# Performance work log

Measured on AMD Instinct MI355X. Metric: run time of the kernel, lower is better.

Reference implementation:

```python
import jax, jax.numpy as jnp
import numpy as np

V, E, L, H, C, NC = 32000, 128, 256, 2048, 256, 10   # vocab, embed, seq_len, ae_hidden, cnn_out/d_model, classes
D_INNER, D_STATE, DT_RANK, D_CONV = 512, 16, 16, 4    # mamba defaults for d_model=256 (expand=2)
B = 64


def setup_inputs() -> dict:
    key = jax.random.key(0)
    ks = jax.random.split(key, 20)
    def rn(k, shape, s=0.02):
        return jax.random.normal(k, shape, jnp.float32) * s
    return {
        "x": jax.random.randint(ks[0], (B, L), 0, V),
        "embed": rn(ks[1], (V, E), 1.0),
        "enc_w1": rn(ks[2], (H, E * L)), "enc_b1": jnp.zeros((H,), jnp.float32),
        "enc_w2": rn(ks[3], (E * L, H)), "enc_b2": jnp.zeros((E * L,), jnp.float32),
        "conv_w": rn(ks[4], (C, E, 5)), "conv_b": jnp.zeros((C,), jnp.float32),
        "in_proj_w": rn(ks[5], (2 * D_INNER, C)),
        "conv1d_w": rn(ks[6], (D_INNER, 1, D_CONV)), "conv1d_b": jnp.zeros((D_INNER,), jnp.float32),
        "x_proj_w": rn(ks[7], (DT_RANK + 2 * D_STATE, D_INNER)),
        "dt_proj_w": rn(ks[8], (D_INNER, DT_RANK), 0.1),
        "dt_proj_b": rn(ks[9], (D_INNER,), 0.1),
        "A_log": jnp.log(jnp.broadcast_to(jnp.arange(1, D_STATE + 1, dtype=jnp.float32), (D_INNER, D_STATE))),
        "D": jnp.ones((D_INNER,), jnp.float32),
        "out_proj_w": rn(ks[10], (C, D_INNER)),
        "fc_w": rn(ks[11], (NC, C)), "fc_b": jnp.zeros((NC,), jnp.float32),
    }


def _mamba(xs, in_proj_w, conv1d_w, conv1d_b, x_proj_w, dt_proj_w, dt_proj_b, A_log, Dp, out_proj_w):
    # xs: (B, Lp, C)
    xz = xs @ in_proj_w.T                                   # (B, Lp, 2*d_inner)
    u, z = jnp.split(xz, 2, axis=-1)
    # causal depthwise conv1d + SiLU
    u_c = u.transpose(0, 2, 1)                              # (B, d_inner, Lp)
    u_c = jnp.pad(u_c, ((0, 0), (0, 0), (D_CONV - 1, 0)))
    u_c = jax.lax.conv_general_dilated(
        u_c, conv1d_w, window_strides=(1,), padding=[(0, 0)],
        dimension_numbers=("NCH", "OIH", "NCH"), feature_group_count=D_INNER)
    u = jax.nn.silu((u_c + conv1d_b[None, :, None]).transpose(0, 2, 1))  # (B, Lp, d_inner)
    # input-dependent dt, B, C
    xdbl = u @ x_proj_w.T
    dt, Bm, Cm = jnp.split(xdbl, [DT_RANK, DT_RANK + D_STATE], axis=-1)
    delta = jax.nn.softplus(dt @ dt_proj_w.T + dt_proj_b)   # (B, Lp, d_inner)
    A = -jnp.exp(A_log)                                     # (d_inner, d_state)
    dA = jnp.exp(jnp.einsum("bld,dn->bldn", delta, A))      # (B, Lp, d_inner, d_state)
    dBu = (delta * u)[..., None] * Bm[:, :, None, :]        # (B, Lp, d_inner, d_state)
    # sequential selective scan over time
    def step(h, inp):
        dA_t, dBu_t, c_t = inp
        h = dA_t * h + dBu_t                                # (B, d_inner, d_state)
        y = jnp.einsum("bdn,bn->bd", h, c_t)
        return h, y
    h0 = jnp.zeros((xs.shape[0], D_INNER, D_STATE), xs.dtype)
    _, ys = jax.lax.scan(step, h0, (dA.transpose(1, 0, 2, 3), dBu.transpose(1, 0, 2, 3), Cm.transpose(1, 0, 2)))
    y = ys.transpose(1, 0, 2) + u * Dp                      # (B, Lp, d_inner)
    y = y * jax.nn.silu(z)
    return y @ out_proj_w.T                                 # (B, Lp, C)


def reference(x, embed, enc_w1, enc_b1, enc_w2, enc_b2, conv_w, conv_b,
              in_proj_w, conv1d_w, conv1d_b, x_proj_w, dt_proj_w, dt_proj_b,
              A_log, D, out_proj_w, fc_w, fc_b):
    b = x.shape[0]
    e = embed[x].reshape(b, -1)                             # (B, E*L)
    h = jax.nn.relu(e @ enc_w1.T + enc_b1)
    h = jax.nn.relu(h @ enc_w2.T + enc_b2)
    h = h.reshape(b, L, E).transpose(0, 2, 1)               # (B, E, L)
    h = jax.lax.conv_general_dilated(h, conv_w, window_strides=(1,), padding=[(2, 2)],
                                     dimension_numbers=("NCH", "OIH", "NCH"))
    h = jax.nn.relu(h + conv_b[None, :, None])              # (B, C, L)
    h = h.reshape(b, C, L // 2, 2).max(axis=-1)             # MaxPool1d(2)
    xs = h.transpose(0, 2, 1)                               # (B, L/2, C)
    y = _mamba(xs, in_proj_w, conv1d_w, conv1d_b, x_proj_w, dt_proj_w, dt_proj_b, A_log, D, out_proj_w)
    return y.mean(axis=1) @ fc_w.T + fc_b                   # (B, NC)
```

## Files before the change

### kernel.cpp

```cpp
#include <hip/hip_runtime.h>
#include <cstddef>
#include <cstdint>

#define B_   64
#define L_   256
#define E_   128
#define H_   2048
#define C_   256
#define LP_  128
#define DI_  512
#define DS_  16

typedef __attribute__((ext_vector_type(8))) short s16x8;
typedef __attribute__((ext_vector_type(4))) float f32x4;

__device__ __forceinline__ uint32_t cvt_pk_bf16(float a, float b) {
  uint32_t r;
  asm("v_cvt_pk_bf16_f32 %0, %1, %2" : "=v"(r) : "v"(a), "v"(b));
  return r;
}

__device__ __forceinline__ void split1(float x, short& h, short& l) {
  uint32_t p = cvt_pk_bf16(x, x);
  float rres = x - __uint_as_float(p << 16);
  uint32_t q = cvt_pk_bf16(rres, rres);
  h = (short)p; l = (short)q;
}

__device__ __forceinline__ void cvt8(const float4& a0, const float4& a1,
                                     s16x8& h, s16x8& l) {
  union { uint32_t u[4]; s16x8 v; } H, L;
  float x[8] = {a0.x, a0.y, a0.z, a0.w, a1.x, a1.y, a1.z, a1.w};
#pragma unroll
  for (int j = 0; j < 4; ++j) {
    uint32_t p = cvt_pk_bf16(x[2*j], x[2*j+1]);
    float r0 = x[2*j]   - __uint_as_float(p << 16);
    float r1 = x[2*j+1] - __uint_as_float(p & 0xFFFF0000u);
    H.u[j] = p;
    L.u[j] = cvt_pk_bf16(r0, r1);
  }
  h = H.v; l = L.v;
}

__global__ __launch_bounds__(256) void embed_k(const int* __restrict__ x,
                                               const float* __restrict__ emb,
                                               short* __restrict__ ehi,
                                               short* __restrict__ elo) {
  int bl = blockIdx.x * 4 + (threadIdx.x >> 6);
  int lane = threadIdx.x & 63;
  int idx = x[bl];
  float2 v = ((const float2*)(emb + (size_t)idx * E_))[lane];
  uint32_t p = cvt_pk_bf16(v.x, v.y);
  float r0 = v.x - __uint_as_float(p << 16);
  float r1 = v.y - __uint_as_float(p & 0xFFFF0000u);
  uint32_t q = cvt_pk_bf16(r0, r1);
  ((uint32_t*)ehi)[(size_t)bl * 64 + lane] = p;
  ((uint32_t*)elo)[(size_t)bl * 64 + lane] = q;
}

__global__ __launch_bounds__(256) void prep_all(
    const float* __restrict__ conv_w, const float* __restrict__ ipw,
    const float* __restrict__ opw,    const float* __restrict__ xpw,
    short* __restrict__ wthi,  short* __restrict__ wtlo,
    short* __restrict__ ipwhi, short* __restrict__ ipwlo,
    short* __restrict__ opwhi, short* __restrict__ opwlo,
    short* __restrict__ xpwhi, short* __restrict__ xpwlo) {
  int blk = blockIdx.x, tid = threadIdx.x;
  if (blk < 640) {
    int k = blk, c = tid, t = k >> 7, e = k & 127;
    float v = conv_w[c * 640 + e * 5 + t];
    short h, l; split1(v, h, l);
    wthi[(size_t)c * 640 + k] = h; wtlo[(size_t)c * 640 + k] = l;
  } else if (blk < 640 + 1024) {
    int n = blk - 640;
    size_t i = (size_t)n * 256 + tid;
    short h, l; split1(ipw[i], h, l);
    ipwhi[i] = h; ipwlo[i] = l;
  } else if (blk < 640 + 1024 + 512) {
    size_t i = (size_t)(blk - 1664) * 256 + tid;
    short h, l; split1(opw[i], h, l);
    opwhi[i] = h; opwlo[i] = l;
  } else {
    int i = (blk - 2176) * 256 + tid;
    int n = i >> 9, k = i & 511;
    float v = (n < 48) ? xpw[n * 512 + k] : 0.0f;
    short h, l; split1(v, h, l);
    xpwhi[i] = h; xpwlo[i] = l;
  }
}

template<int AM, int WM, int EPI>
__global__ __launch_bounds__(256) void gemm_t(
    const void* __restrict__ Aa, const void* __restrict__ Ab,
    const void* __restrict__ Wa, const void* __restrict__ Wb,
    const float* __restrict__ bias,
    float* __restrict__ Cf, short* __restrict__ Chi, short* __restrict__ Clo,
    int M, int N, int K, int kChunk) {
  __shared__ __align__(16) short AhiS[64][40];
  __shared__ __align__(16) short AloS[64][40];
  __shared__ __align__(16) short WhiS[64][40];
  __shared__ __align__(16) short WloS[64][40];

  const int tid = threadIdx.x;
  const int r   = tid >> 2;
  const int seg = (tid & 3) * 8;
  const int lane = tid & 63;
  const int wv   = tid >> 6;
  const int ml   = lane & 15;
  const int quad = lane >> 4;
  const int bn = blockIdx.x * 64, bm = blockIdx.y * 64;
  const int kStart = blockIdx.z * kChunk, kEnd = kStart + kChunk;

  f32x4 acc[4];
#pragma unroll
  for (int nt = 0; nt < 4; ++nt) acc[nt] = (f32x4){0.f, 0.f, 0.f, 0.f};

  auto loadA = [&](int k0, s16x8& h, s16x8& l) {
    if constexpr (AM == 0) {
      const float* Ar = (const float*)Aa + (size_t)(bm + r) * K + seg + k0;
      float4 a0 = *(const float4*)Ar;
      float4 a1 = *(const float4*)(Ar + 4);
      cvt8(a0, a1, h, l);
    } else if constexpr (AM == 1) {
      size_t o = (size_t)(bm + r) * K + seg + k0;
      h = *(const s16x8*)((const short*)Aa + o);
      l = *(const s16x8*)((const short*)Ab + o);
    } else {
      int m = bm + r, bb = m >> 8, lrow = m & 255;
      int k = k0 + seg, t = k >> 7, e = k & 127;
      int ls = lrow + t - 2;
      if (ls >= 0 && ls < 256) {
        size_t o = ((size_t)bb << 15) + ((size_t)ls << 7) + (size_t)e;
        h = *(const s16x8*)((const short*)Aa + o);
        l = *(const s16x8*)((const short*)Ab + o);
      } else {
        h = (s16x8)(short)0; l = (s16x8)(short)0;
      }
    }
  };
  auto loadW = [&](int k0, s16x8& h, s16x8& l) {
    if constexpr (WM == 0) {
      const float* Wr = (const float*)Wa + (size_t)(bn + r) * K + seg + k0;
      float4 w0 = *(const float4*)Wr;
      float4 w1 = *(const float4*)(Wr + 4);
      cvt8(w0, w1, h, l);
    } else {
      size_t o = (size_t)(bn + r) * K + seg + k0;
      h = *(const s16x8*)((const short*)Wa + o);
      l = *(const s16x8*)((const short*)Wb + o);
    }
  };

  s16x8 pAh, pAl, pWh, pWl;
  loadA(kStart, pAh, pAl);
  loadW(kStart, pWh, pWl);

  for (int k0 = kStart; k0 < kEnd; k0 += 32) {
    __syncthreads();
    *(s16x8*)&AhiS[r][seg] = pAh;
    *(s16x8*)&AloS[r][seg] = pAl;
    *(s16x8*)&WhiS[r][seg] = pWh;
    *(s16x8*)&WloS[r][seg] = pWl;
    __syncthreads();
    if (k0 + 32 < kEnd) {
      loadA(k0 + 32, pAh, pAl);
      loadW(k0 + 32, pWh, pWl);
    }
    s16x8 fah = *(const s16x8*)&AhiS[wv * 16 + ml][quad * 8];
    s16x8 fal = *(const s16x8*)&AloS[wv * 16 + ml][quad * 8];
#pragma unroll
    for (int nt = 0; nt < 4; ++nt) {
      s16x8 fwh = *(const s16x8*)&WhiS[nt * 16 + ml][quad * 8];
      s16x8 fwl = *(const s16x8*)&WloS[nt * 16 + ml][quad * 8];
      acc[nt] = __builtin_amdgcn_mfma_f32_16x16x32_bf16(fah, fwh, acc[nt], 0, 0, 0);
      acc[nt] = __builtin_amdgcn_mfma_f32_16x16x32_bf16(fah, fwl, acc[nt], 0, 0, 0);
      acc[nt] = __builtin_amdgcn_mfma_f32_16x16x32_bf16(fal, fwh, acc[nt], 0, 0, 0);
    }
  }

  if constexpr (EPI == 1) {
    float* P = Cf + (size_t)blockIdx.z * ((size_t)M * N);
#pragma unroll
    for (int nt = 0; nt < 4; ++nt) {
      int n = bn + nt * 16 + ml;
#pragma unroll
      for (int i = 0; i < 4; ++i) {
        int m = bm + wv * 16 + quad * 4 + i;
        P[(size_t)m * N + n] = acc[nt][i];
      }
    }
  } else if constexpr (EPI == 0) {
#pragma unroll
    for (int nt = 0; nt < 4; ++nt) {
      int n = bn + nt * 16 + ml;
      float bv = bias ? bias[n] : 0.0f;
#pragma unroll
      for (int i = 0; i < 4; ++i) {
        int m = bm + wv * 16 + quad * 4 + i;
        Cf[(size_t)m * N + n] = acc[nt][i] + bv;
      }
    }
  } else if constexpr (EPI == 2) {
#pragma unroll
    for (int nt = 0; nt < 4; ++nt) {
      int n = bn + nt * 16 + ml;
      float bv = bias[n];
#pragma unroll
      for (int i = 0; i < 4; ++i) {
        int m = bm + wv * 16 + quad * 4 + i;
        float v = acc[nt][i] + bv;
        v = v > 0.0f ? v : 0.0f;
        short hh, ll; split1(v, hh, ll);
        Chi[(size_t)m * N + n] = hh;
        Clo[(size_t)m * N + n] = ll;
      }
    }
  } else {
    int m0 = bm + wv * 16 + quad * 4;
    int bb = m0 >> 8;
    int lb = m0 & 255;
    size_t row0 = ((size_t)bb * 128 + (lb >> 1)) * 256;
#pragma unroll
    for (int nt = 0; nt < 4; ++nt) {
      int n = bn + nt * 16 + ml;
      float bv = bias[n];
      float v0 = fmaxf(acc[nt][0] + bv, 0.0f);
      float v1 = fmaxf(acc[nt][1] + bv, 0.0f);
      float v2 = fmaxf(acc[nt][2] + bv, 0.0f);
      float v3 = fmaxf(acc[nt][3] + bv, 0.0f);
      float p0 = fmaxf(v0, v1), p1 = fmaxf(v2, v3);
      short hh, ll;
      split1(p0, hh, ll);
      Chi[row0 + n] = hh; Clo[row0 + n] = ll;
      split1(p1, hh, ll);
      Chi[row0 + 256 + n] = hh; Clo[row0 + 256 + n] = ll;
    }
  }
}

__global__ __launch_bounds__(256) void reduce_k(const float* __restrict__ P,
                                                const float* __restrict__ bias,
                                                short* __restrict__ hhi,
                                                short* __restrict__ hlo,
                                                int MN, int N, int S) {
  int i = blockIdx.x * 256 + threadIdx.x;
  if (i >= MN) return;
  float s = 0.0f;
  for (int z = 0; z < S; ++z) s += P[(size_t)z * MN + i];
  s += bias[i & (N - 1)];
  s = s > 0.0f ? s : 0.0f;
  short hh, ll; split1(s, hh, ll);
  hhi[i] = hh; hlo[i] = ll;
}

__global__ __launch_bounds__(512) void dwconv_k(const float* __restrict__ xz,
                                                const float* __restrict__ cw,
                                                const float* __restrict__ cb,
                                                float* __restrict__ u2) {
  int m = blockIdx.x;
  int t = m & (LP_ - 1);
  int d = threadIdx.x;
  float4 w = *(const float4*)(cw + d * 4);
  const float* base = xz + (size_t)m * (2 * DI_) + d;
  float pre = cb[d];
  if (t >= 3) {
    pre = fmaf(base[-3 * 2 * DI_], w.x, pre);
    pre = fmaf(base[-2 * 2 * DI_], w.y, pre);
    pre = fmaf(base[-1 * 2 * DI_], w.z, pre);
    pre = fmaf(base[0],            w.w, pre);
  } else {
    const float wv[4] = {w.x, w.y, w.z, w.w};
    for (int j = 0; j < 4; ++j) {
      int tt = t - 3 + j;
      if (tt >= 0) pre = fmaf(base[(j - 3) * 2 * DI_], wv[j], pre);
    }
  }
  float s = pre / (1.0f + __expf(-pre));
  u2[(size_t)m * DI_ + d] = s;
}

__global__ __launch_bounds__(256) void scan_k(const float* __restrict__ u2,
                                              const float* __restrict__ xz,
                                              const float* __restrict__ xdbl,
                                              const float* __restrict__ dtw,
                                              const float* __restrict__ dtb,
                                              const float* __restrict__ A_log,
                                              const float* __restrict__ Dp,
                                              short* __restrict__ yghi,
                                              short* __restrict__ yglo) {
  __shared__ float dls[16][128];
  const int tid = threadIdx.x;
  const int b = blockIdx.x >> 5;
  const int d0 = (blockIdx.x & 31) << 4;
  const size_t mBase = (size_t)b * LP_;

  {
    const int ch = tid >> 4;
    const int t0 = (tid & 15) * 8;
    const int d = d0 + ch;
    const float4* wr = (const float4*)(dtw + d * 16);
    float4 w0 = wr[0], w1 = wr[1], w2 = wr[2], w3 = wr[3];
    float bdt = dtb[d];
#pragma unroll
    for (int j = 0; j < 8; ++j) {
      int t = t0 + j;
      const float4* xr = (const float4*)(xdbl + (mBase + t) * 64);
      float4 x0 = xr[0], x1 = xr[1], x2 = xr[2], x3 = xr[3];
      float a = bdt;
      a = fmaf(w0.x, x0.x, a); a = fmaf(w0.y, x0.y, a);
      a = fmaf(w0.z, x0.z, a); a = fmaf(w0.w, x0.w, a);
      a = fmaf(w1.x, x1.x, a); a = fmaf(w1.y, x1.y, a);
      a = fmaf(w1.z, x1.z, a); a = fmaf(w1.w, x1.w, a);
      a = fmaf(w2.x, x2.x, a); a = fmaf(w2.y, x2.y, a);
      a = fmaf(w2.z, x2.z, a); a = fmaf(w2.w, x2.w, a);
      a = fmaf(w3.x, x3.x, a); a = fmaf(w3.y, x3.y, a);
      a = fmaf(w3.z, x3.z, a); a = fmaf(w3.w, x3.w, a);
      float sp = fmaxf(a, 0.0f) + log1pf(__expf(-fabsf(a)));
      dls[ch][t] = sp;
    }
  }
  __syncthreads();

  const int n = tid & 15;
  const int ch = tid >> 4;
  const int d = d0 + ch;
  float An = -__expf(A_log[d * 16 + n]);
  float Dd = Dp[d];
  float h = 0.0f;
  for (int t = 0; t < LP_; ++t) {
    size_t m = mBase + t;
    float dl = dls[ch][t];
    float uu = u2[m * DI_ + d];
    float Bn = xdbl[m * 64 + 16 + n];
    float Cn = xdbl[m * 64 + 32 + n];
    float dA = __expf(dl * An);
    h = fmaf(dA, h, (dl * uu) * Bn);
    float y = h * Cn;
    y += __shfl_xor(y, 1, 16);
    y += __shfl_xor(y, 2, 16);
    y += __shfl_xor(y, 4, 16);
    y += __shfl_xor(y, 8, 16);
    if (n == 0) {
      float zz = xz[m * (2 * DI_) + DI_ + d];
      float g = zz / (1.0f + __expf(-zz));
      float yv = fmaf(uu, Dd, y) * g;
      short hh, ll; split1(yv, hh, ll);
      yghi[m * DI_ + d] = hh;
      yglo[m * DI_ + d] = ll;
    }
  }
}

__global__ __launch_bounds__(256) void meanfc_k(const float* __restrict__ mout,
                                                const float* __restrict__ fcw,
                                                const float* __restrict__ fcb,
                                                float* __restrict__ out) {
  __shared__ float pooled[256];
  int b = blockIdx.x;
  int c = threadIdx.x;
  float s = 0.0f;
  for (int t = 0; t < LP_; ++t) s += mout[((size_t)b * LP_ + t) * C_ + c];
  pooled[c] = s * (1.0f / 128.0f);
  __syncthreads();
  if (c < 10) {
    float acc = fcb[c];
    for (int k = 0; k < 256; ++k) acc = fmaf(pooled[k], fcw[c * 256 + k], acc);
    out[b * 10 + c] = acc;
  }
}

extern "C" void kernel_launch(void* const* d_in, const int* in_sizes, int n_in,
                              void* d_out, int out_size, void* d_ws, size_t ws_size,
                              hipStream_t stream) {
  const int*   x         = (const int*)d_in[0];
  const float* embed     = (const float*)d_in[1];
  const float* enc_w1    = (const float*)d_in[2];
  const float* enc_b1    = (const float*)d_in[3];
  const float* enc_w2    = (const float*)d_in[4];
  const float* enc_b2    = (const float*)d_in[5];
  const float* conv_w    = (const float*)d_in[6];
  const float* conv_b    = (const float*)d_in[7];
  const float* in_proj_w = (const float*)d_in[8];
  const float* conv1d_w  = (const float*)d_in[9];
  const float* conv1d_b  = (const float*)d_in[10];
  const float* x_proj_w  = (const float*)d_in[11];
  const float* dt_proj_w = (const float*)d_in[12];
  const float* dt_proj_b = (const float*)d_in[13];
  const float* A_log     = (const float*)d_in[14];
  const float* Dp        = (const float*)d_in[15];
  const float* out_proj_w= (const float*)d_in[16];
  const float* fc_w      = (const float*)d_in[17];
  const float* fc_b      = (const float*)d_in[18];
  float* out = (float*)d_out;

  char* ws = (char*)d_ws;
  size_t off = 0;
  auto alloc = [&](size_t bytes) {
    char* p = ws + off;
    off += (bytes + 255) & ~(size_t)255;
    return p;
  };
  short* ehi   = (short*)alloc(2097152ull * 2);
  short* elo   = (short*)alloc(2097152ull * 2);
  float* P     = (float*)alloc(4194304ull * 4);
  short* h1hi  = (short*)alloc(131072ull  * 2);
  short* h1lo  = (short*)alloc(131072ull  * 2);
  short* h2hi  = (short*)alloc(2097152ull * 2);
  short* h2lo  = (short*)alloc(2097152ull * 2);
  short* wthi  = (short*)alloc(163840ull  * 2);
  short* wtlo  = (short*)alloc(163840ull  * 2);
  short* ipwhi = (short*)alloc(262144ull  * 2);
  short* ipwlo = (short*)alloc(262144ull  * 2);
  short* xpwhi = (short*)alloc(32768ull   * 2);
  short* xpwlo = (short*)alloc(32768ull   * 2);
  short* opwhi = (short*)alloc(131072ull  * 2);
  short* opwlo = (short*)alloc(131072ull  * 2);
  short* xshi  = (short*)alloc(2097152ull * 2);
  short* xslo  = (short*)alloc(2097152ull * 2);
  float* xz    = (float*)alloc(8388608ull * 4);
  float* u2    = (float*)alloc(4194304ull * 4);
  float* xdbl  = (float*)alloc(524288ull  * 4);
  short* yghi  = (short*)alloc(4194304ull * 2);
  short* yglo  = (short*)alloc(4194304ull * 2);
  float* mout  = (float*)alloc(2097152ull * 4);
  (void)ws_size; (void)in_sizes; (void)n_in; (void)out_size;

  prep_all<<<2304, 256, 0, stream>>>(conv_w, in_proj_w, out_proj_w, x_proj_w,
                                     wthi, wtlo, ipwhi, ipwlo, opwhi, opwlo,
                                     xpwhi, xpwlo);
  embed_k<<<4096, 256, 0, stream>>>(x, embed, ehi, elo);

  gemm_t<1, 0, 1><<<dim3(32, 1, 32), 256, 0, stream>>>(
      ehi, elo, enc_w1, nullptr, nullptr, P, nullptr, nullptr,
      64, 2048, 32768, 1024);
  reduce_k<<<512, 256, 0, stream>>>(P, enc_b1, h1hi, h1lo, 131072, 2048, 32);

  gemm_t<1, 0, 2><<<dim3(512, 1, 1), 256, 0, stream>>>(
      h1hi, h1lo, enc_w2, nullptr, enc_b2, nullptr, h2hi, h2lo,
      64, 32768, 2048, 2048);

  gemm_t<2, 1, 3><<<dim3(4, 256, 1), 256, 0, stream>>>(
      h2hi, h2lo, wthi, wtlo, conv_b, nullptr, xshi, xslo,
      16384, 256, 640, 640);

  gemm_t<1, 1, 0><<<dim3(16, 128, 1), 256, 0, stream>>>(
      xshi, xslo, ipwhi, ipwlo, nullptr, xz, nullptr, nullptr,
      8192, 1024, 256, 256);

  dwconv_k<<<8192, 512, 0, stream>>>(xz, conv1d_w, conv1d_b, u2);

  gemm_t<0, 1, 0><<<dim3(1, 128, 1), 256, 0, stream>>>(
      u2, nullptr, xpwhi, xpwlo, nullptr, xdbl, nullptr, nullptr,
      8192, 64, 512, 512);

  scan_k<<<2048, 256, 0, stream>>>(u2, xz, xdbl, dt_proj_w, dt_proj_b,
                                   A_log, Dp, yghi, yglo);

  gemm_t<1, 1, 0><<<dim3(4, 128, 1), 256, 0, stream>>>(
      yghi, yglo, opwhi, opwlo, nullptr, mout, nullptr, nullptr,
      8192, 256, 512, 512);

  meanfc_k<<<64, 256, 0, stream>>>(mout, fc_w, fc_b, out);
}
```

Measured before the change: 963.7 us.

## Stage scan inputs in double-buffered shared memory and batch warp reductions

The selective-scan kernel now loads u, z and B/C for 32-timestep chunks into double-buffered shared memory with coalesced vector loads, prefetching the next chunk while the current one is computed. Shuffle reductions are batched over 8 timesteps so the reduction latency is amortized, and outputs are staged in shared memory and written back coalesced. The dt precompute also switches to a strided time mapping and the padded dls array to reduce bank conflicts. This adds more shared memory, more barriers and more register pressure.

```diff
diff --git a/kernel.cpp b/kernel.cpp
--- a/kernel.cpp
+++ b/kernel.cpp
@@ -288,7 +288,13 @@
                                               const float* __restrict__ Dp,
                                               short* __restrict__ yghi,
                                               short* __restrict__ yglo) {
-  __shared__ float dls[16][128];
+  __shared__ float dls[16][132];
+  __shared__ __align__(16) float u2s[2][32][16];
+  __shared__ __align__(16) float zs [2][32][16];
+  __shared__ __align__(16) float bcs[2][32][32];
+  __shared__ short ygs_hi[32][16];
+  __shared__ short ygs_lo[32][16];
+
   const int tid = threadIdx.x;
   const int b = blockIdx.x >> 5;
   const int d0 = (blockIdx.x & 31) << 4;
@@ -296,14 +302,14 @@
 
   {
     const int ch = tid >> 4;
-    const int t0 = (tid & 15) * 8;
+    const int tl = tid & 15;
     const int d = d0 + ch;
     const float4* wr = (const float4*)(dtw + d * 16);
     float4 w0 = wr[0], w1 = wr[1], w2 = wr[2], w3 = wr[3];
     float bdt = dtb[d];
 #pragma unroll
     for (int j = 0; j < 8; ++j) {
-      int t = t0 + j;
+      int t = tl + 16 * j;
       const float4* xr = (const float4*)(xdbl + (mBase + t) * 64);
       float4 x0 = xr[0], x1 = xr[1], x2 = xr[2], x3 = xr[3];
       float a = bdt;
@@ -319,34 +325,81 @@
       dls[ch][t] = sp;
     }
   }
-  __syncthreads();
-
-  const int n = tid & 15;
+
+  const int stt = tid >> 3;
+  const int sjj = tid & 7;
+  {
+    size_t m = mBase + stt;
+    float2 ru  = *(const float2*)(u2 + m * DI_ + d0 + sjj * 2);
+    float2 rz  = *(const float2*)(xz + m * (2 * DI_) + DI_ + d0 + sjj * 2);
+    float4 rbc = *(const float4*)(xdbl + m * 64 + 16 + sjj * 4);
+    *(float2*)&u2s[0][stt][sjj * 2] = ru;
+    *(float2*)&zs [0][stt][sjj * 2] = rz;
+    *(float4*)&bcs[0][stt][sjj * 4] = rbc;
+  }
+
+  const int n  = tid & 15;
   const int ch = tid >> 4;
-  const int d = d0 + ch;
+  const int d  = d0 + ch;
   float An = -__expf(A_log[d * 16 + n]);
   float Dd = Dp[d];
   float h = 0.0f;
-  for (int t = 0; t < LP_; ++t) {
-    size_t m = mBase + t;
-    float dl = dls[ch][t];
-    float uu = u2[m * DI_ + d];
-    float Bn = xdbl[m * 64 + 16 + n];
-    float Cn = xdbl[m * 64 + 32 + n];
-    float dA = __expf(dl * An);
-    h = fmaf(dA, h, (dl * uu) * Bn);
-    float y = h * Cn;
-    y += __shfl_xor(y, 1, 16);
-    y += __shfl_xor(y, 2, 16);
-    y += __shfl_xor(y, 4, 16);
-    y += __shfl_xor(y, 8, 16);
-    if (n == 0) {
-      float zz = xz[m * (2 * DI_) + DI_ + d];
-      float g = zz / (1.0f + __expf(-zz));
-      float yv = fmaf(uu, Dd, y) * g;
-      short hh, ll; split1(yv, hh, ll);
-      yghi[m * DI_ + d] = hh;
-      yglo[m * DI_ + d] = ll;
+
+  for (int c = 0; c < 4; ++c) {
+    const int buf = c & 1;
+    __syncthreads();
+    float2 ru, rz; float4 rbc;
+    const bool pre = (c < 3);
+    if (pre) {
+      size_t m = mBase + (c + 1) * 32 + stt;
+      ru  = *(const float2*)(u2 + m * DI_ + d0 + sjj * 2);
+      rz  = *(const float2*)(xz + m * (2 * DI_) + DI_ + d0 + sjj * 2);
+      rbc = *(const float4*)(xdbl + m * 64 + 16 + sjj * 4);
+    }
+    float y[8];
+#pragma unroll
+    for (int tb = 0; tb < 32; tb += 8) {
+#pragma unroll
+      for (int j = 0; j < 8; ++j) {
+        int tt = tb + j;
+        float dl = dls[ch][c * 32 + tt];
+        float uu = u2s[buf][tt][ch];
+        float Bn = bcs[buf][tt][n];
+        float Cn = bcs[buf][tt][16 + n];
+        float dA = __expf(dl * An);
+        h = fmaf(dA, h, (dl * uu) * Bn);
+        y[j] = h * Cn;
+      }
+#pragma unroll
+      for (int s = 1; s < 16; s <<= 1) {
+#pragma unroll
+        for (int j = 0; j < 8; ++j) y[j] += __shfl_xor(y[j], s, 16);
+      }
+      float my = y[0];
+#pragma unroll
+      for (int j = 1; j < 8; ++j) my = (n == j) ? y[j] : my;
+      if (n < 8) {
+        int tt = tb + n;
+        float uu = u2s[buf][tt][ch];
+        float zz = zs[buf][tt][ch];
+        float g = zz / (1.0f + __expf(-zz));
+        float yv = fmaf(uu, Dd, my) * g;
+        short hh, ll; split1(yv, hh, ll);
+        ygs_hi[tt][ch] = hh;
+        ygs_lo[tt][ch] = ll;
+      }
+    }
+    __syncthreads();
+    {
+      size_t m = mBase + c * 32 + stt;
+      ((uint32_t*)(yghi + m * DI_ + d0))[sjj] = *(uint32_t*)&ygs_hi[stt][sjj * 2];
+      ((uint32_t*)(yglo + m * DI_ + d0))[sjj] = *(uint32_t*)&ygs_lo[stt][sjj * 2];
+    }
+    if (pre) {
+      const int nb = buf ^ 1;
+      *(float2*)&u2s[nb][stt][sjj * 2] = ru;
+      *(float2*)&zs [nb][stt][sjj * 2] = rz;
+      *(float4*)&bcs[nb][stt][sjj * 4] = rbc;
     }
   }
 }
```

After: 839.7 us. 1.15x faster.
